# Optimization experiments

Hardware: AMD Instinct MI355X
Metric: run time of the kernel (lower is better)

Reference implementation:

```python
import jax, jax.numpy as jnp
import numpy as np

NUM_USERS = 100000
NUM_ITEMS = 50000
EMB = 64
NNZ = 4_800_000
N = NUM_USERS + NUM_ITEMS


def setup_inputs() -> dict:
    key = jax.random.key(0)
    k1, k2, k3, k4, k5 = jax.random.split(key, 5)
    row = jax.random.randint(k1, (NNZ,), 0, N, dtype=jnp.int64 if jax.config.jax_enable_x64 else jnp.int32)
    col = jax.random.randint(k2, (NNZ,), 0, N, dtype=row.dtype)
    # normalized adjacency values (positive, ~1/avg_degree scale)
    vals = jax.random.uniform(k3, (NNZ,), dtype=jnp.float32) * (1.0 / 32.0)
    user_emb = jax.random.normal(k4, (NUM_USERS, EMB), dtype=jnp.float32)
    item_emb = jax.random.normal(k5, (NUM_ITEMS, EMB), dtype=jnp.float32)
    return {"row": row, "col": col, "vals": vals,
            "user_emb": user_emb, "item_emb": item_emb, "n_layers": 3}


def reference(row, col, vals, user_emb, item_emb, n_layers):
    # ego_embeddings = cat(user, item)  -> [N, D]
    ego = jnp.concatenate([user_emb, item_emb], axis=0)
    acc = ego  # running sum over layers (layer 0 included)
    for _ in range(n_layers):
        # sparse.mm(norm_adj, ego): gather source rows, scale, scatter-add to dest rows
        ego = jax.ops.segment_sum(vals[:, None] * ego[col], row, num_segments=N)
        acc = acc + ego
    mean_emb = acc / jnp.asarray(n_layers + 1, dtype=acc.dtype)  # mean over layer axis
    return mean_emb[:NUM_USERS], mean_emb[NUM_USERS:]
```

## Files before the change

kernel.cpp:

```cpp
#include <hip/hip_runtime.h>
#include <hip/hip_fp16.h>


#define NUSERS 100000
#define NITEMS 50000
#define NN     150000
#define D      64
#define NNZ_E  4800000

#define NB_BU  74
#define BU_PAD 80
#define NCHUNK 1024
#define CH     4688

__global__ void init_kernel(const float* __restrict__ ue,
                            const float* __restrict__ ie,
                            float* __restrict__ acc,
                            __half* __restrict__ ego) {
    int t = blockIdx.x * blockDim.x + threadIdx.x;
    const int total = NN * (D / 4);
    if (t >= total) return;
    const int user_f4 = NUSERS * (D / 4);
    float4 v;
    if (t < user_f4) v = ((const float4*)ue)[t];
    else             v = ((const float4*)ie)[t - user_f4];
    ((float4*)acc)[t] = v;
    __half2 h01 = __float22half2_rn(make_float2(v.x, v.y));
    __half2 h23 = __float22half2_rn(make_float2(v.z, v.w));
    uint2 packed;
    packed.x = *(unsigned*)&h01;
    packed.y = *(unsigned*)&h23;
    ((uint2*)ego)[t] = packed;
}

__global__ void p1_kernel(const int* __restrict__ row, int* __restrict__ cnt) {
    __shared__ int l[BU_PAD];
    for (int i = threadIdx.x; i < BU_PAD; i += 256) l[i] = 0;
    __syncthreads();
    int b = blockIdx.x;
    int beg = b * CH, end = min(beg + CH, NNZ_E);
    for (int e = beg + threadIdx.x; e < end; e += 256)
        atomicAdd(&l[row[e] >> 11], 1);
    __syncthreads();
    for (int i = threadIdx.x; i < BU_PAD; i += 256) cnt[b * BU_PAD + i] = l[i];
}

__global__ void s1_kernel(const int* __restrict__ cnt,
                          int* __restrict__ woff,
                          int* __restrict__ butot) {
    __shared__ int wsum[16];
    int bu = blockIdx.x;
    int b = threadIdx.x;
    int lane = b & 63;
    int w = b >> 6;
    int d = cnt[b * BU_PAD + bu];
    int incl = d;
    #pragma unroll
    for (int off = 1; off < 64; off <<= 1) {
        int t = __shfl_up(incl, off, 64);
        if (lane >= off) incl += t;
    }
    if (lane == 63) wsum[w] = incl;
    __syncthreads();
    int woffs = 0;
    for (int i = 0; i < w; ++i) woffs += wsum[i];
    woff[b * BU_PAD + bu] = woffs + incl - d;
    if (b == 1023) butot[bu] = woffs + incl;
}

__global__ void s2_kernel(const int* __restrict__ butot, int* __restrict__ bbase) {
    __shared__ int sh[128];
    int t = threadIdx.x;
    sh[t] = (t < NB_BU) ? butot[t] : 0;
    __syncthreads();
    for (int off = 1; off < 128; off <<= 1) {
        int x = (t >= off) ? sh[t - off] : 0;
        __syncthreads();
        sh[t] += x;
        __syncthreads();
    }
    if (t == 0) bbase[0] = 0;
    if (t < NB_BU) bbase[t + 1] = sh[t];
}

__global__ void p2_kernel(const int* __restrict__ row,
                          const int* __restrict__ col,
                          const float* __restrict__ vals,
                          const int* __restrict__ woff,
                          const int* __restrict__ bbase,
                          uint2* __restrict__ rec) {
    __shared__ int cur[BU_PAD];
    int b = blockIdx.x;
    for (int i = threadIdx.x; i < BU_PAD; i += 256) {
        int base = (i < NB_BU) ? bbase[i] : 0;
        cur[i] = base + woff[b * BU_PAD + i];
    }
    __syncthreads();
    int beg = b * CH, end = min(beg + CH, NNZ_E);
    for (int e = beg + threadIdx.x; e < end; e += 256) {
        int r = row[e];
        unsigned code = (unsigned)(vals[e] * 524288.0f + 0.5f);
        code = min(code, 16383u);
        unsigned cv = ((unsigned)col[e] << 14) | code;
        int p = atomicAdd(&cur[r >> 11], 1);
        rec[p] = make_uint2(cv, (unsigned)(r & 2047));
    }
}

__global__ __launch_bounds__(1024) void p3f_kernel(const int* __restrict__ bbase,
                                                   const uint2* __restrict__ rec,
                                                   int* __restrict__ start,
                                                   int* __restrict__ deg,
                                                   unsigned* __restrict__ ecv) {
    __shared__ int lh[2048];
    __shared__ int cur[2048];
    __shared__ int wsum[16];
    int bu = blockIdx.x;
    int beg = bbase[bu], end = bbase[bu + 1];
    int t = threadIdx.x;
    lh[t] = 0;
    lh[t + 1024] = 0;
    __syncthreads();
    for (int i = beg + t; i < end; i += 1024)
        atomicAdd(&lh[rec[i].y], 1);
    __syncthreads();
    int h0 = lh[2 * t], h1 = lh[2 * t + 1];
    int sum2 = h0 + h1;
    int lane = t & 63, w = t >> 6;
    int incl = sum2;
    #pragma unroll
    for (int off = 1; off < 64; off <<= 1) {
        int x = __shfl_up(incl, off, 64);
        if (lane >= off) incl += x;
    }
    if (lane == 63) wsum[w] = incl;
    __syncthreads();
    int woffs = 0;
    for (int i = 0; i < w; ++i) woffs += wsum[i];
    int excl = woffs + incl - sum2;
    cur[2 * t] = excl;
    cur[2 * t + 1] = excl + h0;
    int n0 = (bu << 11) + 2 * t;
    if (n0 < NN) {
        start[n0] = beg + excl;
        deg[n0] = h0;
    }
    if (n0 + 1 < NN) {
        start[n0 + 1] = beg + excl + h0;
        deg[n0 + 1] = h1;
    }
    __syncthreads();
    for (int i = beg + t; i < end; i += 1024) {
        uint2 r = rec[i];
        int p = atomicAdd(&cur[r.y], 1);
        ecv[beg + p] = r.x;
    }
}

__global__ void gather_kernel(const int* __restrict__ start,
                              const int* __restrict__ deg,
                              const unsigned* __restrict__ ecv,
                              const __half* __restrict__ ego,
                              __half* __restrict__ nxt,
                              float* __restrict__ acc,
                              float s, int write_next) {
    int wid = threadIdx.x >> 6;
    int lane = threadIdx.x & 63;
    int n = blockIdx.x * 4 + wid;
    int st = start[n];
    int dg = deg[n];
    int k = lane & 7;
    int g = lane >> 3;
    const float4* ego4 = (const float4*)ego;
    float sum[8] = {0.f, 0.f, 0.f, 0.f, 0.f, 0.f, 0.f, 0.f};
    for (int b = 0; b < dg; b += 64) {
        unsigned cv = (b + lane < dg) ? ecv[st + b + lane] : 0u;
        int m = min(64, dg - b);
        int steps = (m + 7) >> 3;
        for (int j = 0; j < steps; ++j) {
            unsigned cvj = (unsigned)__shfl((int)cv, 8 * j + g, 64);
            int c = (int)(cvj >> 14);
            float v = (float)(cvj & 16383u) * (1.0f / 524288.0f);
            float4 raw = ego4[c * 8 + k];
            const __half2* hp = (const __half2*)&raw;
            float2 f0 = __half22float2(hp[0]);
            float2 f1 = __half22float2(hp[1]);
            float2 f2 = __half22float2(hp[2]);
            float2 f3 = __half22float2(hp[3]);
            sum[0] = fmaf(v, f0.x, sum[0]);
            sum[1] = fmaf(v, f0.y, sum[1]);
            sum[2] = fmaf(v, f1.x, sum[2]);
            sum[3] = fmaf(v, f1.y, sum[3]);
            sum[4] = fmaf(v, f2.x, sum[4]);
            sum[5] = fmaf(v, f2.y, sum[5]);
            sum[6] = fmaf(v, f3.x, sum[6]);
            sum[7] = fmaf(v, f3.y, sum[7]);
        }
    }
    #pragma unroll
    for (int off = 8; off < 64; off <<= 1) {
        #pragma unroll
        for (int i = 0; i < 8; ++i) sum[i] += __shfl_xor(sum[i], off, 64);
    }
    if (g < 2) {
        float4 sv = (g == 0) ? make_float4(sum[0], sum[1], sum[2], sum[3])
                             : make_float4(sum[4], sum[5], sum[6], sum[7]);
        int o = n * 16 + 2 * k + g;
        float4 a = ((float4*)acc)[o];
        a.x = (a.x + sv.x) * s;
        a.y = (a.y + sv.y) * s;
        a.z = (a.z + sv.z) * s;
        a.w = (a.w + sv.w) * s;
        ((float4*)acc)[o] = a;
    }
    if (write_next && g == 0) {
        __half2 h0 = __float22half2_rn(make_float2(sum[0], sum[1]));
        __half2 h1 = __float22half2_rn(make_float2(sum[2], sum[3]));
        __half2 h2 = __float22half2_rn(make_float2(sum[4], sum[5]));
        __half2 h3 = __float22half2_rn(make_float2(sum[6], sum[7]));
        uint4 packed;
        packed.x = *(unsigned*)&h0;
        packed.y = *(unsigned*)&h1;
        packed.z = *(unsigned*)&h2;
        packed.w = *(unsigned*)&h3;
        ((uint4*)nxt)[n * 8 + k] = packed;
    }
}

extern "C" void kernel_launch(void* const* d_in, const int* in_sizes, int n_in,
                              void* d_out, int out_size, void* d_ws, size_t ws_size,
                              hipStream_t stream) {
    const int*   row  = (const int*)d_in[0];
    const int*   col  = (const int*)d_in[1];
    const float* vals = (const float*)d_in[2];
    const float* ue   = (const float*)d_in[3];
    const float* ie   = (const float*)d_in[4];

    float* acc = (float*)d_out;

    char* ws = (char*)d_ws;
    __half*   ego     = (__half*)(ws);
    __half*   nxt     = (__half*)(ws + (size_t)NN * D * 2);
    char*     p       = ws + 2 * (size_t)NN * D * 2;
    int*      start   = (int*)(p);              p += (size_t)NN * 4;
    int*      deg     = (int*)(p);              p += (size_t)NN * 4;
    int*      butot   = (int*)(p);              p += BU_PAD * 4;
    int*      bbase   = (int*)(p);              p += (BU_PAD + 8) * 4;
    int*      cnt     = (int*)(p);              p += (size_t)NCHUNK * BU_PAD * 4;
    int*      woff    = (int*)(p);              p += (size_t)NCHUNK * BU_PAD * 4;
    unsigned* ecv     = (unsigned*)(p);         p += (size_t)NNZ_E * 4;
    uint2*    rec     = (uint2*)(p);

    const int f4_total = NN * (D / 4);
    const int init_blocks = (f4_total + 255) / 256;
    init_kernel<<<init_blocks, 256, 0, stream>>>(ue, ie, acc, ego);

    p1_kernel<<<NCHUNK, 256, 0, stream>>>(row, cnt);
    s1_kernel<<<NB_BU, 1024, 0, stream>>>(cnt, woff, butot);
    s2_kernel<<<1, 128, 0, stream>>>(butot, bbase);
    p2_kernel<<<NCHUNK, 256, 0, stream>>>(row, col, vals, woff, bbase, rec);
    p3f_kernel<<<NB_BU, 1024, 0, stream>>>(bbase, rec, start, deg, ecv);

    const int gather_blocks = NN / 4;
    __half* in  = ego;
    __half* out = nxt;
    for (int layer = 0; layer < 3; ++layer) {
        float s = (layer == 2) ? 0.25f : 1.0f;
        int write_next = (layer < 2) ? 1 : 0;
        gather_kernel<<<gather_blocks, 256, 0, stream>>>(start, deg, ecv, in, out, acc,
                                                         s, write_next);
        __half* tmp = in; in = out; out = tmp;
    }
}
```

Baseline: 576.3 us.

## Use finer 256-row buckets and stage CSR scatter in shared memory

Shrinks row buckets from 2048 to 256 rows, so the final CSR-building kernel launches 586 blocks instead of 74. The histogram and partition kernels now use fewer, larger chunks with 512 threads. The per-bucket scatter writes into a shared-memory staging array and then copies it out to global memory in one coalesced pass, and the count/offset scratch arrays reuse the not-yet-used next-embedding buffer. The aim is better GPU occupancy and less scattered global writing during preprocessing. The trade-off is that each bucket must fit in 16384 edges of shared memory, which holds for uniformly random rows but could overflow on skewed graphs.

```diff
diff --git a/kernel.cpp b/kernel.cpp
--- a/kernel.cpp
+++ b/kernel.cpp
@@ -8,10 +8,11 @@
 #define D      64
 #define NNZ_E  4800000
 
-#define NB_BU  74
-#define BU_PAD 80
-#define NCHUNK 1024
-#define CH     4688
+#define NB_BU  586
+#define BU_PAD 592
+#define NCHUNK 256
+#define CH     18750
+#define STAGE_CAP 16384
 
 __global__ void init_kernel(const float* __restrict__ ue,
                             const float* __restrict__ ie,
@@ -35,25 +36,25 @@
 
 __global__ void p1_kernel(const int* __restrict__ row, int* __restrict__ cnt) {
     __shared__ int l[BU_PAD];
-    for (int i = threadIdx.x; i < BU_PAD; i += 256) l[i] = 0;
+    for (int i = threadIdx.x; i < BU_PAD; i += 512) l[i] = 0;
     __syncthreads();
     int b = blockIdx.x;
     int beg = b * CH, end = min(beg + CH, NNZ_E);
-    for (int e = beg + threadIdx.x; e < end; e += 256)
-        atomicAdd(&l[row[e] >> 11], 1);
-    __syncthreads();
-    for (int i = threadIdx.x; i < BU_PAD; i += 256) cnt[b * BU_PAD + i] = l[i];
+    for (int e = beg + threadIdx.x; e < end; e += 512)
+        atomicAdd(&l[row[e] >> 8], 1);
+    __syncthreads();
+    for (int i = threadIdx.x; i < BU_PAD; i += 512) cnt[b * BU_PAD + i] = l[i];
 }
 
 __global__ void s1_kernel(const int* __restrict__ cnt,
                           int* __restrict__ woff,
                           int* __restrict__ butot) {
-    __shared__ int wsum[16];
+    __shared__ int wsum[4];
     int bu = blockIdx.x;
-    int b = threadIdx.x;
-    int lane = b & 63;
-    int w = b >> 6;
-    int d = cnt[b * BU_PAD + bu];
+    int c = threadIdx.x;
+    int lane = c & 63;
+    int w = c >> 6;
+    int d = cnt[c * BU_PAD + bu];
     int incl = d;
     #pragma unroll
     for (int off = 1; off < 64; off <<= 1) {
@@ -64,16 +65,16 @@
     __syncthreads();
     int woffs = 0;
     for (int i = 0; i < w; ++i) woffs += wsum[i];
-    woff[b * BU_PAD + bu] = woffs + incl - d;
-    if (b == 1023) butot[bu] = woffs + incl;
+    woff[c * BU_PAD + bu] = woffs + incl - d;
+    if (c == 255) butot[bu] = woffs + incl;
 }
 
 __global__ void s2_kernel(const int* __restrict__ butot, int* __restrict__ bbase) {
-    __shared__ int sh[128];
+    __shared__ int sh[1024];
     int t = threadIdx.x;
     sh[t] = (t < NB_BU) ? butot[t] : 0;
     __syncthreads();
-    for (int off = 1; off < 128; off <<= 1) {
+    for (int off = 1; off < 1024; off <<= 1) {
         int x = (t >= off) ? sh[t - off] : 0;
         __syncthreads();
         sh[t] += x;
@@ -91,70 +92,73 @@
                           uint2* __restrict__ rec) {
     __shared__ int cur[BU_PAD];
     int b = blockIdx.x;
-    for (int i = threadIdx.x; i < BU_PAD; i += 256) {
+    for (int i = threadIdx.x; i < BU_PAD; i += 512) {
         int base = (i < NB_BU) ? bbase[i] : 0;
         cur[i] = base + woff[b * BU_PAD + i];
     }
     __syncthreads();
     int beg = b * CH, end = min(beg + CH, NNZ_E);
-    for (int e = beg + threadIdx.x; e < end; e += 256) {
+    for (int e = beg + threadIdx.x; e < end; e += 512) {
         int r = row[e];
         unsigned code = (unsigned)(vals[e] * 524288.0f + 0.5f);
         code = min(code, 16383u);
         unsigned cv = ((unsigned)col[e] << 14) | code;
-        int p = atomicAdd(&cur[r >> 11], 1);
-        rec[p] = make_uint2(cv, (unsigned)(r & 2047));
-    }
-}
-
-__global__ __launch_bounds__(1024) void p3f_kernel(const int* __restrict__ bbase,
-                                                   const uint2* __restrict__ rec,
-                                                   int* __restrict__ start,
-                                                   int* __restrict__ deg,
-                                                   unsigned* __restrict__ ecv) {
-    __shared__ int lh[2048];
-    __shared__ int cur[2048];
-    __shared__ int wsum[16];
+        int p = atomicAdd(&cur[r >> 8], 1);
+        rec[p] = make_uint2(cv, (unsigned)(r & 255));
+    }
+}
+
+__global__ __launch_bounds__(512) void p3f_kernel(const int* __restrict__ bbase,
+                                                  const uint2* __restrict__ rec,
+                                                  int* __restrict__ start,
+                                                  int* __restrict__ deg,
+                                                  unsigned* __restrict__ ecv) {
+    __shared__ unsigned stage[STAGE_CAP];
+    __shared__ int lh[256];
+    __shared__ int cur[256];
+    __shared__ int wsum[4];
     int bu = blockIdx.x;
     int beg = bbase[bu], end = bbase[bu + 1];
     int t = threadIdx.x;
-    lh[t] = 0;
-    lh[t + 1024] = 0;
-    __syncthreads();
-    for (int i = beg + t; i < end; i += 1024)
+    if (t < 256) lh[t] = 0;
+    __syncthreads();
+    for (int i = beg + t; i < end; i += 512)
         atomicAdd(&lh[rec[i].y], 1);
     __syncthreads();
-    int h0 = lh[2 * t], h1 = lh[2 * t + 1];
-    int sum2 = h0 + h1;
+    int h = 0, incl = 0;
     int lane = t & 63, w = t >> 6;
-    int incl = sum2;
-    #pragma unroll
-    for (int off = 1; off < 64; off <<= 1) {
-        int x = __shfl_up(incl, off, 64);
-        if (lane >= off) incl += x;
-    }
-    if (lane == 63) wsum[w] = incl;
-    __syncthreads();
-    int woffs = 0;
-    for (int i = 0; i < w; ++i) woffs += wsum[i];
-    int excl = woffs + incl - sum2;
-    cur[2 * t] = excl;
-    cur[2 * t + 1] = excl + h0;
-    int n0 = (bu << 11) + 2 * t;
-    if (n0 < NN) {
-        start[n0] = beg + excl;
-        deg[n0] = h0;
-    }
-    if (n0 + 1 < NN) {
-        start[n0 + 1] = beg + excl + h0;
-        deg[n0 + 1] = h1;
-    }
-    __syncthreads();
-    for (int i = beg + t; i < end; i += 1024) {
+    if (t < 256) {
+        h = lh[t];
+        incl = h;
+        #pragma unroll
+        for (int off = 1; off < 64; off <<= 1) {
+            int x = __shfl_up(incl, off, 64);
+            if (lane >= off) incl += x;
+        }
+        if (lane == 63) wsum[w] = incl;
+    }
+    __syncthreads();
+    if (t < 256) {
+        int woffs = 0;
+        for (int i = 0; i < w; ++i) woffs += wsum[i];
+        int excl = woffs + incl - h;
+        cur[t] = excl;
+        int n0 = (bu << 8) + t;
+        if (n0 < NN) {
+            start[n0] = beg + excl;
+            deg[n0] = h;
+        }
+    }
+    __syncthreads();
+    for (int i = beg + t; i < end; i += 512) {
         uint2 r = rec[i];
         int p = atomicAdd(&cur[r.y], 1);
-        ecv[beg + p] = r.x;
-    }
+        stage[p] = r.x;
+    }
+    __syncthreads();
+    int n_edges = end - beg;
+    for (int i = t; i < n_edges; i += 512)
+        ecv[beg + i] = stage[i];
 }
 
 __global__ void gather_kernel(const int* __restrict__ start,
@@ -241,13 +245,13 @@
     char* ws = (char*)d_ws;
     __half*   ego     = (__half*)(ws);
     __half*   nxt     = (__half*)(ws + (size_t)NN * D * 2);
+    int*      cnt     = (int*)nxt;
+    int*      woff    = cnt + (size_t)NCHUNK * BU_PAD;
     char*     p       = ws + 2 * (size_t)NN * D * 2;
     int*      start   = (int*)(p);              p += (size_t)NN * 4;
     int*      deg     = (int*)(p);              p += (size_t)NN * 4;
     int*      butot   = (int*)(p);              p += BU_PAD * 4;
     int*      bbase   = (int*)(p);              p += (BU_PAD + 8) * 4;
-    int*      cnt     = (int*)(p);              p += (size_t)NCHUNK * BU_PAD * 4;
-    int*      woff    = (int*)(p);              p += (size_t)NCHUNK * BU_PAD * 4;
     unsigned* ecv     = (unsigned*)(p);         p += (size_t)NNZ_E * 4;
     uint2*    rec     = (uint2*)(p);
 
@@ -255,11 +259,11 @@
     const int init_blocks = (f4_total + 255) / 256;
     init_kernel<<<init_blocks, 256, 0, stream>>>(ue, ie, acc, ego);
 
-    p1_kernel<<<NCHUNK, 256, 0, stream>>>(row, cnt);
-    s1_kernel<<<NB_BU, 1024, 0, stream>>>(cnt, woff, butot);
-    s2_kernel<<<1, 128, 0, stream>>>(butot, bbase);
-    p2_kernel<<<NCHUNK, 256, 0, stream>>>(row, col, vals, woff, bbase, rec);
-    p3f_kernel<<<NB_BU, 1024, 0, stream>>>(bbase, rec, start, deg, ecv);
+    p1_kernel<<<NCHUNK, 512, 0, stream>>>(row, cnt);
+    s1_kernel<<<NB_BU, 256, 0, stream>>>(cnt, woff, butot);
+    s2_kernel<<<1, 1024, 0, stream>>>(butot, bbase);
+    p2_kernel<<<NCHUNK, 512, 0, stream>>>(row, col, vals, woff, bbase, rec);
+    p3f_kernel<<<NB_BU, 512, 0, stream>>>(bbase, rec, start, deg, ecv);
 
     const int gather_blocks = NN / 4;
     __half* in  = ego;
```

Result: faster. 534.1 us (-7.3%).
